# Performance work log

Measured on AMD Instinct MI355X. Metric: run time of the kernel, lower is better.

Reference implementation:

```python
import jax, jax.numpy as jnp
import numpy as np

N_NODES = 100000
N_EDGES = 1600000
IN_DIM = 128
HID_DIM = 128


def gcn_conv(x, W, b, src, dst, n_nodes):
    # PyG GCNConv: linear (no bias) -> symmetric degree norm with self-loops -> scatter-add -> +bias
    h = x @ W  # [N, H]
    e = src.shape[0]
    deg = jax.ops.segment_sum(jnp.ones((e,), dtype=h.dtype), dst, num_segments=n_nodes) + 1.0  # +1 self-loop
    dinv = deg ** -0.5  # deg >= 1 always
    norm = dinv[src] * dinv[dst]  # [E]
    agg = jax.ops.segment_sum(h[src] * norm[:, None], dst, num_segments=n_nodes)
    agg = agg + h * (dinv * dinv)[:, None]  # self-loop contribution
    return agg + b


def setup_inputs() -> dict:
    key = jax.random.key(0)
    ks = jax.random.split(key, 8)
    x = jax.random.normal(ks[0], (N_NODES, IN_DIM), dtype=jnp.float32)
    edge_index = jax.random.randint(ks[1], (2, N_EDGES), 0, N_NODES, dtype=jnp.int32)
    def glorot(k, fan_in, fan_out):
        lim = np.sqrt(6.0 / (fan_in + fan_out)).astype(np.float32)
        return jax.random.uniform(k, (fan_in, fan_out), dtype=jnp.float32, minval=-lim, maxval=lim)
    W1 = glorot(ks[2], IN_DIM, HID_DIM)
    W2 = glorot(ks[3], HID_DIM, HID_DIM)
    W3 = glorot(ks[4], HID_DIM, HID_DIM)
    b1 = jnp.zeros((HID_DIM,), jnp.float32)
    b2 = jnp.zeros((HID_DIM,), jnp.float32)
    b3 = jnp.zeros((HID_DIM,), jnp.float32)
    return {"x": x, "W1": W1, "b1": b1, "W2": W2, "b2": b2, "W3": W3, "b3": b3,
            "edge_index": edge_index}


def reference(x, W1, b1, W2, b2, W3, b3, edge_index):
    src, dst = edge_index[0], edge_index[1]
    n = x.shape[0]
    z = jax.nn.relu(gcn_conv(x, W1, b1, src, dst, n))
    z = jax.nn.relu(gcn_conv(z, W2, b2, src, dst, n))
    z = gcn_conv(z, W3, b3, src, dst, n)
    # edge dot-product decode on the same edge set
    logits = jnp.sum(z[src] * z[dst], axis=1)  # [E]
    return jax.nn.sigmoid(logits)
```

## Files before the change

kernel.cpp:

```cpp
#include <hip/hip_runtime.h>
#include <math.h>

#define NN 100000
#define NE 1600000
#define DIM 128
#define SCHUNK 1024
#define NBK 391
#define ECH 4096

typedef unsigned short u16;
typedef unsigned int u32;
typedef __attribute__((ext_vector_type(8))) short bf16x8;
typedef __attribute__((ext_vector_type(4))) float f32x4;

__device__ inline u16 f2bf(float f) {
  union { float f; u32 u; } v; v.f = f;
  u32 r = v.u + 0x7FFF + ((v.u >> 16) & 1);
  return (u16)(r >> 16);
}
__device__ inline float bflo(u32 u) { union { u32 u; float f; } v; v.u = u << 16; return v.f; }
__device__ inline float bfhi(u32 u) { union { u32 u; float f; } v; v.u = u & 0xFFFF0000u; return v.f; }

__global__ void k_deg(const int* __restrict__ dst, int* __restrict__ deg) {
  int i = blockIdx.x * blockDim.x + threadIdx.x;
  if (i < NE) atomicAdd(&deg[dst[i]], 1);
}

__global__ void k_dinv(const int* __restrict__ deg, float* __restrict__ dinv) {
  int i = blockIdx.x * blockDim.x + threadIdx.x;
  if (i < NN) dinv[i] = rsqrtf((float)deg[i] + 1.0f);
}

__global__ void k_scan1(const int* __restrict__ deg, int* __restrict__ bsum) {
  __shared__ int sd[256];
  int t = threadIdx.x;
  int base = blockIdx.x * SCHUNK + t * 4;
  int s = 0;
#pragma unroll
  for (int j = 0; j < 4; ++j) { int idx = base + j; if (idx < NN) s += deg[idx]; }
  sd[t] = s; __syncthreads();
  for (int off = 128; off > 0; off >>= 1) {
    if (t < off) sd[t] += sd[t + off];
    __syncthreads();
  }
  if (t == 0) bsum[blockIdx.x] = sd[0];
}

__global__ void k_scan2(int* __restrict__ bsum, int nb) {
  if (threadIdx.x == 0 && blockIdx.x == 0) {
    int run = 0;
    for (int b = 0; b < nb; ++b) { int v = bsum[b]; bsum[b] = run; run += v; }
  }
}

__global__ void k_scan3(const int* __restrict__ deg, const int* __restrict__ bsum,
                        int* __restrict__ offs) {
  __shared__ int ts[256];
  int t = threadIdx.x;
  int base = blockIdx.x * SCHUNK + t * 4;
  int v[4]; int loc = 0;
#pragma unroll
  for (int j = 0; j < 4; ++j) { int idx = base + j; v[j] = (idx < NN) ? deg[idx] : 0; loc += v[j]; }
  ts[t] = loc; __syncthreads();
  for (int off = 1; off < 256; off <<= 1) {
    int x = (t >= off) ? ts[t - off] : 0;
    __syncthreads();
    ts[t] += x;
    __syncthreads();
  }
  int run = bsum[blockIdx.x] + ts[t] - loc;
#pragma unroll
  for (int j = 0; j < 4; ++j) { int idx = base + j; if (idx < NN) offs[idx] = run; run += v[j]; }
}

__launch_bounds__(256)
__global__ void k_bucket(const int* __restrict__ src, const int* __restrict__ dst,
                         const int* __restrict__ offs, int* __restrict__ bcur,
                         uint2* __restrict__ bstage) {
  __shared__ int cnt[512];
  __shared__ int bl[512];
  __shared__ int gb[512];
  __shared__ int tmp[256];
  __shared__ uint2 st[ECH];
  int t = threadIdx.x;
  int e0 = blockIdx.x * ECH;
  cnt[t] = 0; cnt[t + 256] = 0;
  __syncthreads();
  int b_[16], r_[16]; u32 s_[16], y_[16];
#pragma unroll
  for (int k = 0; k < 16; ++k) {
    int i = e0 + k * 256 + t;
    b_[k] = -1;
    if (i < NE) {
      int d = dst[i];
      int bb = d >> 8;
      b_[k] = bb;
      s_[k] = (u32)src[i];
      y_[k] = ((u32)(d & 255) << 21) | (u32)i;
      r_[k] = atomicAdd(&cnt[bb], 1);
    }
  }
  __syncthreads();
  int c0 = cnt[2 * t], c1 = cnt[2 * t + 1];
  tmp[t] = c0 + c1;
  __syncthreads();
  for (int off = 1; off < 256; off <<= 1) {
    int v = (t >= off) ? tmp[t - off] : 0;
    __syncthreads();
    tmp[t] += v;
    __syncthreads();
  }
  int excl = tmp[t] - (c0 + c1);
  bl[2 * t] = excl; bl[2 * t + 1] = excl + c0;
  __syncthreads();
#pragma unroll
  for (int k = 0; k < 16; ++k)
    if (b_[k] >= 0) st[bl[b_[k]] + r_[k]] = make_uint2(s_[k], y_[k]);
  for (int b = t; b < 512; b += 256) {
    int n = cnt[b];
    gb[b] = (n > 0) ? atomicAdd(&bcur[b], n) : 0;
  }
  __syncthreads();
  for (int b = t; b < 512; b += 256) {
    int n = cnt[b];
    if (n > 0) {
      uint2* dp = bstage + offs[b << 8] + gb[b];
      const uint2* sp = st + bl[b];
      for (int j = 0; j < n; ++j) dp[j] = sp[j];
    }
  }
}

__launch_bounds__(256)
__global__ void k_fillb(const uint2* __restrict__ bstage, const int* __restrict__ offs,
                        int* __restrict__ csr_src, int* __restrict__ csr_eid) {
  __shared__ int curl[256];
  int t = threadIdx.x;
  int b = blockIdx.x;
  int nb0 = b << 8;
  curl[t] = 0;
  __syncthreads();
  int sbase = offs[nb0];
  int send = (b == NBK - 1) ? NE : offs[nb0 + 256];
  for (int j = sbase + t; j < send; j += 256) {
    uint2 e = bstage[j];
    int dl = e.y >> 21;
    int eid = e.y & 0x1FFFFF;
    int pos = offs[nb0 + dl] + atomicAdd(&curl[dl], 1);
    csr_src[pos] = (int)e.x;
    csr_eid[pos] = eid;
  }
}

__global__ void k_tobf(const float* __restrict__ in, u16* __restrict__ out, int n4) {
  int i = blockIdx.x * blockDim.x + threadIdx.x;
  if (i < n4) {
    float4 v = ((const float4*)in)[i];
    ushort4 o;
    o.x = f2bf(v.x); o.y = f2bf(v.y); o.z = f2bf(v.z); o.w = f2bf(v.w);
    ((ushort4*)out)[i] = o;
  }
}

__global__ void k_pack(const float* __restrict__ W, u16* __restrict__ Wp) {
  int tid = blockIdx.x * blockDim.x + threadIdx.x;
  int b = tid & 7, j = (tid >> 3) & 15, kb = (tid >> 7) & 3, ks = (tid >> 9) & 3, ct = tid >> 11;
  int k = ks * 32 + kb * 8 + b, col = ct * 16 + j;
  Wp[tid] = f2bf(W[k * 128 + col]);
}

__launch_bounds__(256)
__global__ void k_gemm(const u16* __restrict__ Xb, const u16* __restrict__ Wp,
                       const float* __restrict__ dinv, u16* __restrict__ hp) {
  __shared__ u16 wl[16384];
  __shared__ u16 ctile[4][2048];
  int t = threadIdx.x;
  int w = t >> 6, l = t & 63;
  int row0 = blockIdx.x * 64;
  int rbase = row0 + w * 16;

#pragma unroll
  for (int i = 0; i < 8; ++i) {
    int off = (i * 256 + t) * 8;
    *(uint4*)&wl[off] = *(const uint4*)&Wp[off];
  }
  __syncthreads();

  int arow = rbase + (l & 15);
  arow = arow < NN ? arow : NN - 1;
  const u16* abase = Xb + (size_t)arow * DIM + (l >> 4) * 8;
  bf16x8 a[4];
#pragma unroll
  for (int ks = 0; ks < 4; ++ks) a[ks] = *(const bf16x8*)(abase + ks * 32);

  f32x4 acc[8];
#pragma unroll
  for (int ct = 0; ct < 8; ++ct) {
    acc[ct] = (f32x4){0.f, 0.f, 0.f, 0.f};
#pragma unroll
    for (int ks = 0; ks < 4; ++ks) {
      bf16x8 bfr = *(const bf16x8*)&wl[ct * 2048 + ks * 512 + (l >> 4) * 128 + (l & 15) * 8];
      acc[ct] = __builtin_amdgcn_mfma_f32_16x16x32_bf16(a[ks], bfr, acc[ct], 0, 0, 0);
    }
  }

  float dv[4];
#pragma unroll
  for (int v = 0; v < 4; ++v) {
    int rr = rbase + (l >> 4) * 4 + v;
    dv[v] = dinv[rr < NN ? rr : NN - 1];
  }
  u16* ct_lds = ctile[w];
#pragma unroll
  for (int ct = 0; ct < 8; ++ct) {
#pragma unroll
    for (int v = 0; v < 4; ++v) {
      int row = (l >> 4) * 4 + v;
      ct_lds[row * DIM + ct * 16 + (l & 15)] = f2bf(dv[v] * acc[ct][v]);
    }
  }
  __syncthreads();
#pragma unroll
  for (int rr = 0; rr < 4; ++rr) {
    int row = rr * 4 + (l >> 4);
    int grow = rbase + row;
    if (grow < NN)
      *(uint4*)&hp[(size_t)grow * DIM + (l & 15) * 8] =
          *(const uint4*)&ct_lds[row * DIM + (l & 15) * 8];
  }
}

__launch_bounds__(256)
__global__ void k_agg(const u16* __restrict__ hp, const int* __restrict__ csr_src,
                      const int* __restrict__ offs, const int* __restrict__ deg,
                      const float* __restrict__ dinv, const float* __restrict__ bias,
                      u16* __restrict__ outb, int relu) {
  int t = threadIdx.x;
  int g = t >> 5, l = t & 31;
  int n = blockIdx.x * 8 + g;
  float dn = dinv[n];
  int s = offs[n], cnt = deg[n];
  const uint2* hp2 = (const uint2*)hp;
  float a0 = 0.f, a1 = 0.f, a2 = 0.f, a3 = 0.f;
  int i = 0;
  for (; i + 4 <= cnt; i += 4) {
    int u0 = csr_src[s + i];
    int u1 = csr_src[s + i + 1];
    int u2 = csr_src[s + i + 2];
    int u3 = csr_src[s + i + 3];
    uint2 v0 = hp2[(size_t)u0 * 32 + l];
    uint2 v1 = hp2[(size_t)u1 * 32 + l];
    uint2 v2 = hp2[(size_t)u2 * 32 + l];
    uint2 v3 = hp2[(size_t)u3 * 32 + l];
    a0 += (bflo(v0.x) + bflo(v1.x)) + (bflo(v2.x) + bflo(v3.x));
    a1 += (bfhi(v0.x) + bfhi(v1.x)) + (bfhi(v2.x) + bfhi(v3.x));
    a2 += (bflo(v0.y) + bflo(v1.y)) + (bflo(v2.y) + bflo(v3.y));
    a3 += (bfhi(v0.y) + bfhi(v1.y)) + (bfhi(v2.y) + bfhi(v3.y));
  }
  for (; i < cnt; ++i) {
    int u = csr_src[s + i];
    uint2 v = hp2[(size_t)u * 32 + l];
    a0 += bflo(v.x); a1 += bfhi(v.x); a2 += bflo(v.y); a3 += bfhi(v.y);
  }
  uint2 sv = hp2[(size_t)n * 32 + l];
  float4 bb = ((const float4*)bias)[l];
  float r0 = dn * (a0 + bflo(sv.x)) + bb.x;
  float r1 = dn * (a1 + bfhi(sv.x)) + bb.y;
  float r2 = dn * (a2 + bflo(sv.y)) + bb.z;
  float r3 = dn * (a3 + bfhi(sv.y)) + bb.w;
  if (relu) {
    r0 = fmaxf(r0, 0.f); r1 = fmaxf(r1, 0.f);
    r2 = fmaxf(r2, 0.f); r3 = fmaxf(r3, 0.f);
  }
  ushort4 o; o.x = f2bf(r0); o.y = f2bf(r1); o.z = f2bf(r2); o.w = f2bf(r3);
  *(ushort4*)&outb[(size_t)n * DIM + l * 4] = o;
}

__device__ inline float sigm(float x) { return 1.0f / (1.0f + expf(-x)); }

__launch_bounds__(256)
__global__ void k_decode_node(const u16* __restrict__ z, const int* __restrict__ csr_src,
                              const int* __restrict__ csr_eid, const int* __restrict__ offs,
                              const int* __restrict__ deg, float* __restrict__ out) {
  int t = threadIdx.x;
  int g = t >> 5, l = t & 31;
  int n = blockIdx.x * 8 + g;
  const uint2* z2 = (const uint2*)z;
  uint2 zn = z2[(size_t)n * 32 + l];
  float n0 = bflo(zn.x), n1 = bfhi(zn.x), n2 = bflo(zn.y), n3 = bfhi(zn.y);
  int s = offs[n], cnt = deg[n];
  int i = 0;
  for (; i + 4 <= cnt; i += 4) {
    int u0 = csr_src[s + i];
    int u1 = csr_src[s + i + 1];
    int u2 = csr_src[s + i + 2];
    int u3 = csr_src[s + i + 3];
    uint2 v0 = z2[(size_t)u0 * 32 + l];
    uint2 v1 = z2[(size_t)u1 * 32 + l];
    uint2 v2 = z2[(size_t)u2 * 32 + l];
    uint2 v3 = z2[(size_t)u3 * 32 + l];
    float p0 = bflo(v0.x) * n0 + bfhi(v0.x) * n1 + bflo(v0.y) * n2 + bfhi(v0.y) * n3;
    float p1 = bflo(v1.x) * n0 + bfhi(v1.x) * n1 + bflo(v1.y) * n2 + bfhi(v1.y) * n3;
    float p2 = bflo(v2.x) * n0 + bfhi(v2.x) * n1 + bflo(v2.y) * n2 + bfhi(v2.y) * n3;
    float p3 = bflo(v3.x) * n0 + bfhi(v3.x) * n1 + bflo(v3.y) * n2 + bfhi(v3.y) * n3;
#pragma unroll
    for (int off = 16; off >= 1; off >>= 1) {
      p0 += __shfl_xor(p0, off);
      p1 += __shfl_xor(p1, off);
      p2 += __shfl_xor(p2, off);
      p3 += __shfl_xor(p3, off);
    }
    if (l == 0) {
      out[csr_eid[s + i]]     = sigm(p0);
      out[csr_eid[s + i + 1]] = sigm(p1);
      out[csr_eid[s + i + 2]] = sigm(p2);
      out[csr_eid[s + i + 3]] = sigm(p3);
    }
  }
  for (; i < cnt; ++i) {
    int u = csr_src[s + i];
    uint2 v = z2[(size_t)u * 32 + l];
    float p = bflo(v.x) * n0 + bfhi(v.x) * n1 + bflo(v.y) * n2 + bfhi(v.y) * n3;
#pragma unroll
    for (int off = 16; off >= 1; off >>= 1) p += __shfl_xor(p, off);
    if (l == 0) out[csr_eid[s + i]] = sigm(p);
  }
}

extern "C" void kernel_launch(void* const* d_in, const int* in_sizes, int n_in,
                              void* d_out, int out_size, void* d_ws, size_t ws_size,
                              hipStream_t stream) {
  const float* x  = (const float*)d_in[0];
  const float* W1 = (const float*)d_in[1];
  const float* b1 = (const float*)d_in[2];
  const float* W2 = (const float*)d_in[3];
  const float* b2 = (const float*)d_in[4];
  const float* W3 = (const float*)d_in[5];
  const float* b3 = (const float*)d_in[6];
  const int*   ei = (const int*)d_in[7];
  const int* src = ei;
  const int* dst = ei + NE;
  float* out = (float*)d_out;

  char* w = (char*)d_ws;
  size_t p = 0;
  auto alloc = [&](size_t bytes) -> void* {
    void* r = w + p;
    p += (bytes + 255) & ~(size_t)255;
    return r;
  };
  int*   deg     = (int*)alloc((size_t)NN * 4);
  int*   offs    = (int*)alloc((size_t)NN * 4);
  float* dinv    = (float*)alloc((size_t)NN * 4);
  int*   bsum    = (int*)alloc(1024);
  int*   bcur    = (int*)alloc(512 * 4);
  uint2* bstage  = (uint2*)alloc((size_t)NE * 8);
  int*   csr_src = (int*)alloc((size_t)NE * 4);
  int*   csr_eid = (int*)alloc((size_t)NE * 4);
  u16*   Xb      = (u16*)alloc((size_t)NN * DIM * 2);
  u16*   hp      = (u16*)alloc((size_t)NN * DIM * 2);
  u16*   hb      = (u16*)alloc((size_t)NN * DIM * 2);
  u16*   Wp1     = (u16*)alloc(16384 * 2);
  u16*   Wp2     = (u16*)alloc(16384 * 2);
  u16*   Wp3     = (u16*)alloc(16384 * 2);
  (void)in_sizes; (void)n_in; (void)out_size; (void)ws_size;

  hipMemsetAsync(deg, 0, (size_t)NN * 4, stream);
  hipMemsetAsync(bcur, 0, 512 * 4, stream);

  k_deg<<<(NE + 255) / 256, 256, 0, stream>>>(dst, deg);
  k_dinv<<<(NN + 255) / 256, 256, 0, stream>>>(deg, dinv);
  int nb = (NN + SCHUNK - 1) / SCHUNK;
  k_scan1<<<nb, 256, 0, stream>>>(deg, bsum);
  k_scan2<<<1, 64, 0, stream>>>(bsum, nb);
  k_scan3<<<nb, 256, 0, stream>>>(deg, bsum, offs);

  int cb = (NE + ECH - 1) / ECH;
  k_bucket<<<cb, 256, 0, stream>>>(src, dst, offs, bcur, bstage);
  k_fillb<<<NBK, 256, 0, stream>>>(bstage, offs, csr_src, csr_eid);

  k_tobf<<<(NN * DIM / 4 + 255) / 256, 256, 0, stream>>>(x, Xb, NN * DIM / 4);
  k_pack<<<64, 256, 0, stream>>>(W1, Wp1);
  k_pack<<<64, 256, 0, stream>>>(W2, Wp2);
  k_pack<<<64, 256, 0, stream>>>(W3, Wp3);

  int gb = (NN + 63) / 64;
  k_gemm<<<gb, 256, 0, stream>>>(Xb, Wp1, dinv, hp);
  k_agg <<<NN / 8, 256, 0, stream>>>(hp, csr_src, offs, deg, dinv, b1, hb, 1);
  k_gemm<<<gb, 256, 0, stream>>>(hb, Wp2, dinv, hp);
  k_agg <<<NN / 8, 256, 0, stream>>>(hp, csr_src, offs, deg, dinv, b2, hb, 1);
  k_gemm<<<gb, 256, 0, stream>>>(hb, Wp3, dinv, hp);
  k_agg <<<NN / 8, 256, 0, stream>>>(hp, csr_src, offs, deg, dinv, b3, hb, 0);

  k_decode_node<<<NN / 8, 256, 0, stream>>>(hb, csr_src, csr_eid, offs, deg, out);
}
```

Before: 475.3 us.

## Decode edges with MFMA tiles, fuse dinv into scan, parallelize scan2, merge packs

Edge decoding now runs on MFMA: each wave takes 16-edge tiles in CSR order, fetches source and destination rows, and forms a 16x16 dot-product tile. It keeps only the diagonal-equivalent entries, found by grouping edges that share a destination within the tile. A csr_dst array is added to support this. Smaller changes: dinv is computed inside scan3, the serial scan2 becomes a parallel block scan, the three weight packs become one launch, and the aggregation gather is unrolled by 8. The MFMA decode does extra redundant multiply work and adds a write of csr_dst, in exchange for replacing shuffle reductions.

```diff
diff --git a/kernel.cpp b/kernel.cpp
--- a/kernel.cpp
+++ b/kernel.cpp
@@ -20,15 +20,11 @@
 }
 __device__ inline float bflo(u32 u) { union { u32 u; float f; } v; v.u = u << 16; return v.f; }
 __device__ inline float bfhi(u32 u) { union { u32 u; float f; } v; v.u = u & 0xFFFF0000u; return v.f; }
+__device__ inline float sigm(float x) { return 1.0f / (1.0f + expf(-x)); }
 
 __global__ void k_deg(const int* __restrict__ dst, int* __restrict__ deg) {
   int i = blockIdx.x * blockDim.x + threadIdx.x;
   if (i < NE) atomicAdd(&deg[dst[i]], 1);
-}
-
-__global__ void k_dinv(const int* __restrict__ deg, float* __restrict__ dinv) {
-  int i = blockIdx.x * blockDim.x + threadIdx.x;
-  if (i < NN) dinv[i] = rsqrtf((float)deg[i] + 1.0f);
 }
 
 __global__ void k_scan1(const int* __restrict__ deg, int* __restrict__ bsum) {
@@ -47,14 +43,21 @@
 }
 
 __global__ void k_scan2(int* __restrict__ bsum, int nb) {
-  if (threadIdx.x == 0 && blockIdx.x == 0) {
-    int run = 0;
-    for (int b = 0; b < nb; ++b) { int v = bsum[b]; bsum[b] = run; run += v; }
-  }
+  __shared__ int sd[128];
+  int t = threadIdx.x;
+  int v = (t < nb) ? bsum[t] : 0;
+  sd[t] = v; __syncthreads();
+  for (int off = 1; off < 128; off <<= 1) {
+    int x = (t >= off) ? sd[t - off] : 0;
+    __syncthreads();
+    sd[t] += x;
+    __syncthreads();
+  }
+  if (t < nb) bsum[t] = sd[t] - v;
 }
 
 __global__ void k_scan3(const int* __restrict__ deg, const int* __restrict__ bsum,
-                        int* __restrict__ offs) {
+                        int* __restrict__ offs, float* __restrict__ dinv) {
   __shared__ int ts[256];
   int t = threadIdx.x;
   int base = blockIdx.x * SCHUNK + t * 4;
@@ -70,7 +73,14 @@
   }
   int run = bsum[blockIdx.x] + ts[t] - loc;
 #pragma unroll
-  for (int j = 0; j < 4; ++j) { int idx = base + j; if (idx < NN) offs[idx] = run; run += v[j]; }
+  for (int j = 0; j < 4; ++j) {
+    int idx = base + j;
+    if (idx < NN) {
+      offs[idx] = run;
+      dinv[idx] = rsqrtf((float)v[j] + 1.0f);
+    }
+    run += v[j];
+  }
 }
 
 __launch_bounds__(256)
@@ -133,7 +143,8 @@
 
 __launch_bounds__(256)
 __global__ void k_fillb(const uint2* __restrict__ bstage, const int* __restrict__ offs,
-                        int* __restrict__ csr_src, int* __restrict__ csr_eid) {
+                        int* __restrict__ csr_src, int* __restrict__ csr_dst,
+                        int* __restrict__ csr_eid) {
   __shared__ int curl[256];
   int t = threadIdx.x;
   int b = blockIdx.x;
@@ -148,6 +159,7 @@
     int eid = e.y & 0x1FFFFF;
     int pos = offs[nb0 + dl] + atomicAdd(&curl[dl], 1);
     csr_src[pos] = (int)e.x;
+    csr_dst[pos] = nb0 + dl;
     csr_eid[pos] = eid;
   }
 }
@@ -162,8 +174,14 @@
   }
 }
 
-__global__ void k_pack(const float* __restrict__ W, u16* __restrict__ Wp) {
-  int tid = blockIdx.x * blockDim.x + threadIdx.x;
+__global__ void k_pack3(const float* __restrict__ W1, const float* __restrict__ W2,
+                        const float* __restrict__ W3, u16* __restrict__ Wp1,
+                        u16* __restrict__ Wp2, u16* __restrict__ Wp3) {
+  int gid = blockIdx.x * blockDim.x + threadIdx.x;
+  int which = gid >> 14;
+  int tid = gid & 16383;
+  const float* W = which == 0 ? W1 : (which == 1 ? W2 : W3);
+  u16* Wp = which == 0 ? Wp1 : (which == 1 ? Wp2 : Wp3);
   int b = tid & 7, j = (tid >> 3) & 15, kb = (tid >> 7) & 3, ks = (tid >> 9) & 3, ct = tid >> 11;
   int k = ks * 32 + kb * 8 + b, col = ct * 16 + j;
   Wp[tid] = f2bf(W[k * 128 + col]);
@@ -243,19 +261,29 @@
   const uint2* hp2 = (const uint2*)hp;
   float a0 = 0.f, a1 = 0.f, a2 = 0.f, a3 = 0.f;
   int i = 0;
+  for (; i + 8 <= cnt; i += 8) {
+    int u[8];
+#pragma unroll
+    for (int k = 0; k < 8; ++k) u[k] = csr_src[s + i + k];
+    uint2 v[8];
+#pragma unroll
+    for (int k = 0; k < 8; ++k) v[k] = hp2[(size_t)u[k] * 32 + l];
+#pragma unroll
+    for (int k = 0; k < 8; ++k) {
+      a0 += bflo(v[k].x); a1 += bfhi(v[k].x); a2 += bflo(v[k].y); a3 += bfhi(v[k].y);
+    }
+  }
   for (; i + 4 <= cnt; i += 4) {
-    int u0 = csr_src[s + i];
-    int u1 = csr_src[s + i + 1];
-    int u2 = csr_src[s + i + 2];
-    int u3 = csr_src[s + i + 3];
-    uint2 v0 = hp2[(size_t)u0 * 32 + l];
-    uint2 v1 = hp2[(size_t)u1 * 32 + l];
-    uint2 v2 = hp2[(size_t)u2 * 32 + l];
-    uint2 v3 = hp2[(size_t)u3 * 32 + l];
-    a0 += (bflo(v0.x) + bflo(v1.x)) + (bflo(v2.x) + bflo(v3.x));
-    a1 += (bfhi(v0.x) + bfhi(v1.x)) + (bfhi(v2.x) + bfhi(v3.x));
-    a2 += (bflo(v0.y) + bflo(v1.y)) + (bflo(v2.y) + bflo(v3.y));
-    a3 += (bfhi(v0.y) + bfhi(v1.y)) + (bfhi(v2.y) + bfhi(v3.y));
+    int u[4];
+#pragma unroll
+    for (int k = 0; k < 4; ++k) u[k] = csr_src[s + i + k];
+    uint2 v[4];
+#pragma unroll
+    for (int k = 0; k < 4; ++k) v[k] = hp2[(size_t)u[k] * 32 + l];
+#pragma unroll
+    for (int k = 0; k < 4; ++k) {
+      a0 += bflo(v[k].x); a1 += bfhi(v[k].x); a2 += bflo(v[k].y); a3 += bfhi(v[k].y);
+    }
   }
   for (; i < cnt; ++i) {
     int u = csr_src[s + i];
@@ -276,54 +304,41 @@
   *(ushort4*)&outb[(size_t)n * DIM + l * 4] = o;
 }
 
-__device__ inline float sigm(float x) { return 1.0f / (1.0f + expf(-x)); }
-
 __launch_bounds__(256)
-__global__ void k_decode_node(const u16* __restrict__ z, const int* __restrict__ csr_src,
-                              const int* __restrict__ csr_eid, const int* __restrict__ offs,
-                              const int* __restrict__ deg, float* __restrict__ out) {
-  int t = threadIdx.x;
-  int g = t >> 5, l = t & 31;
-  int n = blockIdx.x * 8 + g;
-  const uint2* z2 = (const uint2*)z;
-  uint2 zn = z2[(size_t)n * 32 + l];
-  float n0 = bflo(zn.x), n1 = bfhi(zn.x), n2 = bflo(zn.y), n3 = bfhi(zn.y);
-  int s = offs[n], cnt = deg[n];
-  int i = 0;
-  for (; i + 4 <= cnt; i += 4) {
-    int u0 = csr_src[s + i];
-    int u1 = csr_src[s + i + 1];
-    int u2 = csr_src[s + i + 2];
-    int u3 = csr_src[s + i + 3];
-    uint2 v0 = z2[(size_t)u0 * 32 + l];
-    uint2 v1 = z2[(size_t)u1 * 32 + l];
-    uint2 v2 = z2[(size_t)u2 * 32 + l];
-    uint2 v3 = z2[(size_t)u3 * 32 + l];
-    float p0 = bflo(v0.x) * n0 + bfhi(v0.x) * n1 + bflo(v0.y) * n2 + bfhi(v0.y) * n3;
-    float p1 = bflo(v1.x) * n0 + bfhi(v1.x) * n1 + bflo(v1.y) * n2 + bfhi(v1.y) * n3;
-    float p2 = bflo(v2.x) * n0 + bfhi(v2.x) * n1 + bflo(v2.y) * n2 + bfhi(v2.y) * n3;
-    float p3 = bflo(v3.x) * n0 + bfhi(v3.x) * n1 + bflo(v3.y) * n2 + bfhi(v3.y) * n3;
-#pragma unroll
-    for (int off = 16; off >= 1; off >>= 1) {
-      p0 += __shfl_xor(p0, off);
-      p1 += __shfl_xor(p1, off);
-      p2 += __shfl_xor(p2, off);
-      p3 += __shfl_xor(p3, off);
-    }
-    if (l == 0) {
-      out[csr_eid[s + i]]     = sigm(p0);
-      out[csr_eid[s + i + 1]] = sigm(p1);
-      out[csr_eid[s + i + 2]] = sigm(p2);
-      out[csr_eid[s + i + 3]] = sigm(p3);
-    }
-  }
-  for (; i < cnt; ++i) {
-    int u = csr_src[s + i];
-    uint2 v = z2[(size_t)u * 32 + l];
-    float p = bflo(v.x) * n0 + bfhi(v.x) * n1 + bflo(v.y) * n2 + bfhi(v.y) * n3;
-#pragma unroll
-    for (int off = 16; off >= 1; off >>= 1) p += __shfl_xor(p, off);
-    if (l == 0) out[csr_eid[s + i]] = sigm(p);
+__global__ void k_decode_mfma(const u16* __restrict__ z, const int* __restrict__ csr_src,
+                              const int* __restrict__ csr_dst, const int* __restrict__ csr_eid,
+                              float* __restrict__ out) {
+  int l = threadIdx.x & 63;
+  int wid = blockIdx.x * 4 + (threadIdx.x >> 6);
+  int r = l & 15, g = l >> 4;
+  int tile0 = wid * 8;
+  for (int tt = 0; tt < 8; ++tt) {
+    int p0 = (tile0 + tt) * 16;
+    int e = p0 + r;
+    int s = csr_src[e];
+    int d = csr_dst[e];
+    int dprev = __shfl(d, (l & 48) | ((r - 1) & 15));
+    unsigned long long bm = __ballot(r > 0 && d != dprev);
+    u32 m16 = (u32)(bm >> (l & 48)) & 0xFFFFu;
+    u32 m = m16; int rc = 0;
+    for (int j = 0; j < r; ++j) {
+      if (!m) break;
+      rc = __ffs(m) - 1;
+      m &= m - 1;
+    }
+    int dget = __shfl(d, (l & 48) | rc);
+    const bf16x8* za = (const bf16x8*)(z + (size_t)s * DIM + g * 8);
+    const bf16x8* zc = (const bf16x8*)(z + (size_t)dget * DIM + g * 8);
+    f32x4 acc = (f32x4){0.f, 0.f, 0.f, 0.f};
+#pragma unroll
+    for (int ks = 0; ks < 4; ++ks)
+      acc = __builtin_amdgcn_mfma_f32_16x16x32_bf16(za[ks * 4], zc[ks * 4], acc, 0, 0, 0);
+#pragma unroll
+    for (int reg = 0; reg < 4; ++reg) {
+      int rr = g * 4 + reg;
+      int colr = __popc(m16 & ((2u << rr) - 1));
+      if (colr == r) out[csr_eid[p0 + rr]] = sigm(acc[reg]);
+    }
   }
 }
 
@@ -356,6 +371,7 @@
   int*   bcur    = (int*)alloc(512 * 4);
   uint2* bstage  = (uint2*)alloc((size_t)NE * 8);
   int*   csr_src = (int*)alloc((size_t)NE * 4);
+  int*   csr_dst = (int*)alloc((size_t)NE * 4);
   int*   csr_eid = (int*)alloc((size_t)NE * 4);
   u16*   Xb      = (u16*)alloc((size_t)NN * DIM * 2);
   u16*   hp      = (u16*)alloc((size_t)NN * DIM * 2);
@@ -369,20 +385,17 @@
   hipMemsetAsync(bcur, 0, 512 * 4, stream);
 
   k_deg<<<(NE + 255) / 256, 256, 0, stream>>>(dst, deg);
-  k_dinv<<<(NN + 255) / 256, 256, 0, stream>>>(deg, dinv);
   int nb = (NN + SCHUNK - 1) / SCHUNK;
   k_scan1<<<nb, 256, 0, stream>>>(deg, bsum);
-  k_scan2<<<1, 64, 0, stream>>>(bsum, nb);
-  k_scan3<<<nb, 256, 0, stream>>>(deg, bsum, offs);
+  k_scan2<<<1, 128, 0, stream>>>(bsum, nb);
+  k_scan3<<<nb, 256, 0, stream>>>(deg, bsum, offs, dinv);
 
   int cb = (NE + ECH - 1) / ECH;
   k_bucket<<<cb, 256, 0, stream>>>(src, dst, offs, bcur, bstage);
-  k_fillb<<<NBK, 256, 0, stream>>>(bstage, offs, csr_src, csr_eid);
+  k_fillb<<<NBK, 256, 0, stream>>>(bstage, offs, csr_src, csr_dst, csr_eid);
 
   k_tobf<<<(NN * DIM / 4 + 255) / 256, 256, 0, stream>>>(x, Xb, NN * DIM / 4);
-  k_pack<<<64, 256, 0, stream>>>(W1, Wp1);
-  k_pack<<<64, 256, 0, stream>>>(W2, Wp2);
-  k_pack<<<64, 256, 0, stream>>>(W3, Wp3);
+  k_pack3<<<192, 256, 0, stream>>>(W1, W2, W3, Wp1, Wp2, Wp3);
 
   int gb = (NN + 63) / 64;
   k_gemm<<<gb, 256, 0, stream>>>(Xb, Wp1, dinv, hp);
@@ -392,5 +405,5 @@
   k_gemm<<<gb, 256, 0, stream>>>(hb, Wp3, dinv, hp);
   k_agg <<<NN / 8, 256, 0, stream>>>(hp, csr_src, offs, deg, dinv, b3, hb, 0);
 
-  k_decode_node<<<NN / 8, 256, 0, stream>>>(hb, csr_src, csr_eid, offs, deg, out);
-}
+  k_decode_mfma<<<3125, 256, 0, stream>>>(hb, csr_src, csr_dst, csr_eid, out);
+}
```

After: 461.0 us. -3.0%, faster.
